# Kernel tuning notes

Measured on AMD Instinct MI355X. Metric: run time of the kernel, lower is better.

The kernel has to match this reference:

```python
import jax, jax.numpy as jnp
import numpy as np

B, C, D, H = 128, 8, 1024, 8
K_RANGE = (2, 3, 4, 5)


def setup_inputs() -> dict:
    key = jax.random.key(0)
    ks = jax.random.split(key, 10)
    s = 0.02
    return {
        "x": jax.random.normal(ks[0], (B, D), jnp.float32),
        # per-K prototype groups, shape (nb_classes, K, embed_dim) as in get_prototype_group()
        "p2": jax.random.normal(ks[1], (C, 2, D), jnp.float32),
        "p3": jax.random.normal(ks[2], (C, 3, D), jnp.float32),
        "p4": jax.random.normal(ks[3], (C, 4, D), jnp.float32),
        "p5": jax.random.normal(ks[4], (C, 5, D), jnp.float32),
        # per-class attention Block params (stacked over class axis)
        "ln_g": jnp.ones((C, D), jnp.float32),
        "ln_b": jnp.zeros((C, D), jnp.float32),
        "w_qkv": jax.random.normal(ks[5], (C, 3 * D, D), jnp.float32) * s,
        "b_qkv": jnp.zeros((C, 3 * D), jnp.float32),
        "w_proj": jax.random.normal(ks[6], (C, D, D), jnp.float32) * s,
        "b_proj": jnp.zeros((C, D), jnp.float32),
        # cls head
        "w_cls": jax.random.normal(ks[7], (C, D), jnp.float32) * s,
        "b_cls": jnp.zeros((C,), jnp.float32),
    }


def _proto_group(x, pg):
    """x: (B,D); pg: (C,K,D). Returns nearest proto (B,D), per-sample class group (B,K,D), class ids (B,)."""
    Cc, K, d = pg.shape
    flat = pg.reshape(Cc * K, d)
    # squared L2 distances (argmin identical to torch.cdist p=2 argmin)
    d2 = (jnp.sum(x * x, axis=1, keepdims=True)
          - 2.0 * (x @ flat.T)
          + jnp.sum(flat * flat, axis=1))
    idx = jnp.argmin(d2, axis=1)          # (B,)
    cls = idx // K                        # (B,)
    return flat[idx], pg[cls], cls


def _vicreg(x, nearest, proto_space, sim_c=25.0, std_c=25.0, cov_c=1.0):
    # sim: pull x toward its nearest prototype in every K-group
    repr_loss = jnp.mean((x[:, None, :] - nearest) ** 2)
    # std over batch of prototype space, unbiased var, eps=1e-4
    std = jnp.sqrt(jnp.var(proto_space, axis=0, ddof=1) + 1e-4)   # (S,D)
    std_loss = jnp.mean(jax.nn.relu(1.0 - std))
    # covariance of centered flattened prototype space
    ps = proto_space - jnp.mean(proto_space, axis=0)
    P = ps.reshape(-1, ps.shape[-1])                              # (B*S, D)
    cov = P.T @ P / (P.shape[0] - 1)
    cov_loss = ((cov ** 2).sum() - (jnp.diagonal(cov) ** 2).sum()) / ps.shape[-1]
    return sim_c * repr_loss + std_c * std_loss + cov_c * cov_loss


def _forward(x, p2, p3, p4, p5, ln_g, ln_b, w_qkv, b_qkv, w_proj, b_proj, w_cls, b_cls):
    groups = (p2, p3, p4, p5)
    nearest_list, space_list, cls = [], [], None
    for pg in groups:
        n, sp, cls = _proto_group(x, pg)   # cls kept from LAST group, as in torch code
        nearest_list.append(n)
        space_list.append(sp)
    nearest = jnp.stack(nearest_list, axis=1)     # (B, len(K_range), D)
    proto_space = jnp.concatenate(space_list, 1)  # (B, sum(K_range), D)

    vcr = _vicreg(x, nearest, proto_space)

    # per-class attention Block: LayerNorm -> MHA -> residual, vectorized over class axis c
    S = proto_space.shape[1]
    mu = proto_space.mean(-1, keepdims=True)
    var = proto_space.var(-1, keepdims=True)
    xn = (proto_space - mu) * jax.lax.rsqrt(var + 1e-5)               # (B,S,D)
    h = xn[None] * ln_g[:, None, None, :] + ln_b[:, None, None, :]    # (C,B,S,D)

    qkv = jnp.einsum('cbsd,cfd->cbsf', h, w_qkv) + b_qkv[:, None, None, :]
    dh = D // H
    qkv = qkv.reshape(C, B, S, 3, H, dh).transpose(3, 0, 1, 4, 2, 5)  # (3,C,B,H,S,dh)
    q, k, v = qkv[0] * (dh ** -0.5), qkv[1], qkv[2]
    attn = jax.nn.softmax(jnp.einsum('cbhqe,cbhke->cbhqk', q, k), axis=-1)
    o = jnp.einsum('cbhqk,cbhke->cbhqe', attn, v)                     # (C,B,H,S,dh)
    o = o.transpose(0, 1, 3, 2, 4).reshape(C, B, S, D)
    out = jnp.einsum('cbsd,ced->cbse', o, w_proj) + b_proj[:, None, None, :]
    attended = proto_space[None] + out                                # (C,B,S,D)

    # route each sample through the block of its (last-group) assigned class
    cond = attended[cls, jnp.arange(B)]                               # (B,S,D)
    cond = cond / jnp.maximum(jnp.linalg.norm(cond, axis=2, keepdims=True), 1e-12)
    pooled = cond.mean(1)                                             # (B,D)
    logits = pooled @ w_cls.T + b_cls
    return logits, vcr


def reference(x, p2, p3, p4, p5, ln_g, ln_b, w_qkv, b_qkv, w_proj, b_proj, w_cls, b_cls):
    return _forward(x, p2, p3, p4, p5, ln_g, ln_b, w_qkv, b_qkv, w_proj, b_proj, w_cls, b_cls)
```

## Files before the change

kernel.cpp:

```cpp
#include <hip/hip_runtime.h>
#include <math.h>

#define NB 128
#define ND 1024
#define NS 14
#define NDH 128

typedef float f32x4 __attribute__((ext_vector_type(4)));
typedef short bf16x8 __attribute__((ext_vector_type(8)));
typedef unsigned int u32x4 __attribute__((ext_vector_type(4)));

__device__ __forceinline__ unsigned short f2bf(float v) {
  unsigned int u = __builtin_bit_cast(unsigned int, v);
  return (unsigned short)((u + 0x7FFFu + ((u >> 16) & 1u)) >> 16);
}
__device__ __forceinline__ float bf2f(unsigned short u) {
  return __builtin_bit_cast(float, (unsigned int)u << 16);
}

__device__ __forceinline__ bf16x8 pack_bv(float4 w0, float4 w1) {
  unsigned int u0, u1, u2, u3;
  asm("v_cvt_pk_bf16_f32 %0, %1, %2" : "=v"(u0) : "v"(w0.x), "v"(w0.y));
  asm("v_cvt_pk_bf16_f32 %0, %1, %2" : "=v"(u1) : "v"(w0.z), "v"(w0.w));
  asm("v_cvt_pk_bf16_f32 %0, %1, %2" : "=v"(u2) : "v"(w1.x), "v"(w1.y));
  asm("v_cvt_pk_bf16_f32 %0, %1, %2" : "=v"(u3) : "v"(w1.z), "v"(w1.w));
  u32x4 u = {u0, u1, u2, u3};
  return __builtin_bit_cast(bf16x8, u);
}

__device__ __forceinline__ void s_decomp(int s, int& g, int& k) {
  if (s < 2)      { g = 0; k = s; }
  else if (s < 5) { g = 1; k = s - 2; }
  else if (s < 9) { g = 2; k = s - 5; }
  else            { g = 3; k = s - 9; }
}
__device__ __forceinline__ const float* grp_ptr(int g, const float* p2, const float* p3,
                                                const float* p4, const float* p5) {
  return g == 0 ? p2 : g == 1 ? p3 : g == 2 ? p4 : p5;
}
__device__ __forceinline__ int grp_base(int g) { return g == 0 ? 0 : g == 1 ? 16 : g == 2 ? 40 : 72; }
__device__ __forceinline__ int grp_k(int g) { return g + 2; }

__global__ __launch_bounds__(256) void k_ln_assign(
    const float* __restrict__ x,
    const float* __restrict__ p2, const float* __restrict__ p3,
    const float* __restrict__ p4, const float* __restrict__ p5,
    const float* __restrict__ ln_g, const float* __restrict__ ln_b,
    const float* __restrict__ w_proj, unsigned short* __restrict__ wpf,
    unsigned short* __restrict__ hbf2, float* __restrict__ pall,
    int* __restrict__ cls, int* __restrict__ rows_g, float* __restrict__ minv)
{
  int bid = blockIdx.x, t = threadIdx.x;
  if (bid >= 240) {
    int idxT = (bid - 240) * 256 + t;
    int c = idxT >> 17;
    int rem = idxT & 131071;
    int col = rem >> 7, kq = rem & 127;
    const float* src = w_proj + (((size_t)c * 1024 + col) << 10) + kq * 8;
    float4 w0 = *(const float4*)(src);
    float4 w1 = *(const float4*)(src + 4);
    bf16x8 v = pack_bv(w0, w1);
    size_t dst = ((((size_t)c * 64 + (col >> 4)) * 32 + (kq >> 2)) << 9)
               + ((kq & 3) * 16 + (col & 15)) * 8;
    *(bf16x8*)(wpf + dst) = v;
    return;
  }
  __shared__ __align__(16) float xs[ND];
  float4* xs4 = (float4*)xs;
  if (bid < 112) {
    int r = bid;
    const float* pp; int idx;
    if (r < 16)      { pp = p2; idx = r; }
    else if (r < 40) { pp = p3; idx = r - 16; }
    else if (r < 72) { pp = p4; idx = r - 40; }
    else             { pp = p5; idx = r - 72; }
    const float4* row4 = (const float4*)(pp + (size_t)idx * ND);
    float4 v = row4[t];
    xs4[t] = v;
    float s1 = v.x + v.y + v.z + v.w;
    float s2 = v.x * v.x + v.y * v.y + v.z * v.z + v.w * v.w;
    __shared__ float ra[256], rb[256];
    ra[t] = s1; rb[t] = s2; __syncthreads();
    for (int o = 128; o > 0; o >>= 1) { if (t < o) { ra[t] += ra[t + o]; rb[t] += rb[t + o]; } __syncthreads(); }
    __shared__ float mu, rstd;
    if (t == 0) {
      float m = ra[0] * (1.f / 1024.f);
      float var = rb[0] * (1.f / 1024.f) - m * m;
      mu = m; rstd = rsqrtf(var + 1e-5f);
    }
    __syncthreads();
    ((float4*)(pall + (size_t)r * ND))[t] = xs4[t];
    float4 xv = xs4[t];
    float nx = (xv.x - mu) * rstd, ny = (xv.y - mu) * rstd,
          nz = (xv.z - mu) * rstd, nw = (xv.w - mu) * rstd;
    int d0 = t * 4;
    int m = r >> 4, rr = r & 15;
    int kblk = d0 >> 5, qq = (d0 >> 3) & 3, e0 = d0 & 7;
    size_t fidx = (size_t)kblk * 3584 + m * 512 + (qq * 16 + rr) * 8 + e0;
#pragma unroll
    for (int c = 0; c < 8; ++c) {
      float4 g = ((const float4*)(ln_g + (size_t)c * ND))[t];
      float4 bb = ((const float4*)(ln_b + (size_t)c * ND))[t];
      ushort4 u;
      u.x = f2bf(nx * g.x + bb.x); u.y = f2bf(ny * g.y + bb.y);
      u.z = f2bf(nz * g.z + bb.z); u.w = f2bf(nw * g.w + bb.w);
      *(ushort4*)&hbf2[(size_t)c * 114688 + fidx] = u;
    }
  } else {
    int b = bid - 112;
    __shared__ float d2s[112];
    __shared__ int cls_s[4];
    const float4* xg4 = (const float4*)(x + (size_t)b * ND);
    xs4[t] = xg4[t];
    __syncthreads();
    int j = t >> 1, half = t & 1;
    if (j < 112) {
      const float* pp; int idx;
      if (j < 16)      { pp = p2; idx = j; }
      else if (j < 40) { pp = p3; idx = j - 16; }
      else if (j < 72) { pp = p4; idx = j - 40; }
      else             { pp = p5; idx = j - 72; }
      const float4* pr4 = (const float4*)(pp + (size_t)idx * ND);
      float acc = 0.f;
      int d0 = half * 128;
#pragma unroll 8
      for (int d = d0; d < d0 + 128; ++d) {
        float4 a = xs4[d], p = pr4[d];
        float dx = a.x - p.x, dy = a.y - p.y, dz = a.z - p.z, dw = a.w - p.w;
        acc += dx * dx + dy * dy + dz * dz + dw * dw;
      }
      acc += __shfl_xor(acc, 1, 2);
      if (half == 0) d2s[j] = acc;
    }
    __syncthreads();
    if (t < 4) {
      int base = grp_base(t), kg = grp_k(t), cnt = 8 * kg;
      float mv = d2s[base]; int mi = 0;
      for (int jj = 1; jj < cnt; ++jj) { float v = d2s[base + jj]; if (v < mv) { mv = v; mi = jj; } }
      int c = mi / kg;
      cls[b * 4 + t] = c; cls_s[t] = c;
      minv[b * 4 + t] = mv;
    }
    __syncthreads();
    if (t < NS) {
      int g, k; s_decomp(t, g, k);
      rows_g[b * NS + t] = grp_base(g) + cls_s[g] * grp_k(g) + k;
    }
  }
}

__global__ __launch_bounds__(256, 4) void k_qkv_prep(
    const unsigned short* __restrict__ hbf2, const float* __restrict__ w_qkv,
    const float* __restrict__ b_qkv, unsigned short* __restrict__ qkv_bf,
    const int* __restrict__ cls, const float* __restrict__ minv,
    int* __restrict__ counts, int* __restrict__ ccnt, int* __restrict__ order,
    int* __restrict__ posof, int* __restrict__ chunkidx, int* __restrict__ chunk_c,
    int* __restrict__ chunk_lo, int* __restrict__ chunkN, float* __restrict__ scal)
{
  __shared__ __align__(16) char smem[32768];
  int bid = blockIdx.x, t = threadIdx.x;
  if (bid == 0) {
    __shared__ int cnt_s[32];
    __shared__ int cc_s[8];
    __shared__ float red[128];
    if (t < 32) cnt_s[t] = 0;
    if (t < 8) cc_s[t] = 0;
    if (t < 4) scal[t] = 0.f;
    __syncthreads();
    if (t < 128) {
      int c3;
#pragma unroll
      for (int g = 0; g < 4; ++g) {
        int c = cls[t * 4 + g];
        atomicAdd(&cnt_s[g * 8 + c], 1);
        if (g == 3) c3 = c;
      }
      int pos = atomicAdd(&cc_s[c3], 1);
      order[c3 * 128 + pos] = t;
      posof[t] = pos;
      red[t] = minv[t * 4 + 0] + minv[t * 4 + 1] + minv[t * 4 + 2] + minv[t * 4 + 3];
    }
    __syncthreads();
    for (int o = 64; o > 0; o >>= 1) { if (t < o) red[t] += red[t + o]; __syncthreads(); }
    if (t == 0) {
      scal[0] = red[0];
      int T = 0;
      for (int c = 0; c < 8; ++c) {
        chunkidx[c] = T;
        int nch = (cc_s[c] + 15) >> 4;
        for (int j = 0; j < nch; ++j) { chunk_c[T] = c; chunk_lo[T] = j * 16; ++T; }
      }
      chunkN[0] = T;
    }
    if (t < 32) counts[t] = cnt_s[t];
    if (t < 8) ccnt[t] = cc_s[t];
    return;
  }
  int qb = bid - 1;
  int c = qb / 192, xb = qb - c * 192;
  int col0 = xb * 16;
  unsigned short* Wl = (unsigned short*)smem;
  {
    const float* Wbase = w_qkv + ((size_t)c * 3072 + col0) * ND;
    int k0 = t * 4;
    int ksq = t >> 6, kblk = (t >> 3) & 7, qq = (t >> 1) & 3, e0 = (t & 1) * 4;
    int sw = ((kblk & 3) << 2) + qq;
    int ebase = ((ksq * 8 + kblk) * 64 + qq * 16) * 8 + e0;
#pragma unroll
    for (int j = 0; j < 16; ++j) {
      float4 w = *(const float4*)(Wbase + (size_t)j * ND + k0);
      unsigned int u0, u1;
      asm("v_cvt_pk_bf16_f32 %0, %1, %2" : "=v"(u0) : "v"(w.x), "v"(w.y));
      asm("v_cvt_pk_bf16_f32 %0, %1, %2" : "=v"(u1) : "v"(w.z), "v"(w.w));
      unsigned int* dst = (unsigned int*)&Wl[ebase + (j ^ sw) * 8];
      dst[0] = u0; dst[1] = u1;
    }
  }
  __syncthreads();
  int lane = t & 63, ks = t >> 6;
  int r16 = lane & 15, q = lane >> 4;
  const unsigned short* Hp = hbf2 + (size_t)c * 114688 + (size_t)(ks * 8) * 3584 + lane * 8;
  f32x4 acc[7] = {};
#pragma unroll
  for (int i = 0; i < 8; ++i) {
    int sr = ((i & 3) << 2) + q;
    bf16x8 bv = *(const bf16x8*)&Wl[(((ks * 8 + i) * 64) + q * 16 + (r16 ^ sr)) * 8];
    const unsigned short* hk = Hp + (size_t)i * 3584;
#pragma unroll
    for (int m = 0; m < 7; ++m) {
      bf16x8 av = *(const bf16x8*)(hk + m * 512);
      acc[m] = __builtin_amdgcn_mfma_f32_16x16x32_bf16(av, bv, acc[m], 0, 0, 0);
    }
  }
  __syncthreads();
  float* lred = (float*)smem;
  if (ks) {
#pragma unroll
    for (int m = 0; m < 7; ++m)
      *(f32x4*)&lred[((ks - 1) * 7 + m) * 256 + lane * 4] = acc[m];
  }
  __syncthreads();
  if (ks == 0) {
    int col = col0 + r16;
    float bq = b_qkv[(size_t)c * 3072 + col];
#pragma unroll
    for (int m = 0; m < 7; ++m) {
      f32x4 s0 = acc[m];
#pragma unroll
      for (int sk = 0; sk < 3; ++sk)
        s0 += *(const f32x4*)&lred[(sk * 7 + m) * 256 + lane * 4];
#pragma unroll
      for (int r = 0; r < 4; ++r) {
        int row = m * 16 + q * 4 + r;
        qkv_bf[((size_t)c * 112 + row) * 3072 + col] = f2bf(s0[r] + bq);
      }
    }
  }
}

__global__ __launch_bounds__(256) void k_attn_stats(
    const unsigned short* __restrict__ qkv_bf, const int* __restrict__ cls,
    const int* __restrict__ rows_g, const int* __restrict__ posof,
    const int* __restrict__ chunkidx, unsigned short* __restrict__ obf2,
    const float* __restrict__ p2, const float* __restrict__ p3,
    const float* __restrict__ p4, const float* __restrict__ p5,
    const int* __restrict__ counts, float* __restrict__ M, float* __restrict__ scal)
{
  int bid = blockIdx.x, t = threadIdx.x;
  if (bid < 1024) {
    __shared__ __align__(16) float qs[NS * NDH], ks2[NS * NDH], vs[NS * NDH];
    __shared__ float sc[NS * NS];
    __shared__ int rg[NS];
    int h = bid & 7, b = bid >> 3;
    if (t < NS) rg[t] = rows_g[b * NS + t];
    __syncthreads();
    int cp = cls[b * 4 + 3];
    int pos = posof[b];
    size_t gbase = (size_t)(chunkidx[cp] + (pos >> 4)) * 229376;
    int slot = pos & 15;
    const float scale = 0.08838834764831843f;
    for (int i = t; i < NS * 32; i += 256) {
      int s = i >> 5, e4 = (i & 31) * 4;
      size_t base = ((size_t)cp * 112 + rg[s]) * 3072 + h * NDH + e4;
      ushort4 uq = *(const ushort4*)&qkv_bf[base];
      ushort4 uk = *(const ushort4*)&qkv_bf[base + 1024];
      ushort4 uv = *(const ushort4*)&qkv_bf[base + 2048];
      int o = s * NDH + e4;
      qs[o]     = bf2f(uq.x) * scale; qs[o + 1] = bf2f(uq.y) * scale;
      qs[o + 2] = bf2f(uq.z) * scale; qs[o + 3] = bf2f(uq.w) * scale;
      ks2[o]     = bf2f(uk.x); ks2[o + 1] = bf2f(uk.y);
      ks2[o + 2] = bf2f(uk.z); ks2[o + 3] = bf2f(uk.w);
      vs[o]     = bf2f(uv.x); vs[o + 1] = bf2f(uv.y);
      vs[o + 2] = bf2f(uv.z); vs[o + 3] = bf2f(uv.w);
    }
    __syncthreads();
    if (t < NS * NS) {
      int si = t / NS, sj = t - (t / NS) * NS;
      const float4* qa = (const float4*)&qs[si * NDH];
      const float4* kb = (const float4*)&ks2[sj * NDH];
      float acc = 0.f;
#pragma unroll 8
      for (int e4 = 0; e4 < 32; ++e4) {
        float4 a = qa[e4], k4 = kb[e4];
        acc += a.x * k4.x + a.y * k4.y + a.z * k4.z + a.w * k4.w;
      }
      sc[t] = acc;
    }
    __syncthreads();
    if (t < NS) {
      float mx = -1e30f;
      for (int j = 0; j < NS; ++j) mx = fmaxf(mx, sc[t * NS + j]);
      float e_[NS]; float sum = 0.f;
      for (int j = 0; j < NS; ++j) { float e = expf(sc[t * NS + j] - mx); e_[j] = e; sum += e; }
      float inv = 1.f / sum;
      for (int j = 0; j < NS; ++j) sc[t * NS + j] = e_[j] * inv;
    }
    __syncthreads();
    for (int i = t; i < NS * 32; i += 256) {
      int s = i >> 5, e4 = i & 31;
      float4 a = {0.f, 0.f, 0.f, 0.f};
#pragma unroll
      for (int j = 0; j < NS; ++j) {
        float w = sc[s * NS + j];
        float4 v4 = ((const float4*)&vs[j * NDH])[e4];
        a.x += w * v4.x; a.y += w * v4.y; a.z += w * v4.z; a.w += w * v4.w;
      }
      int row = slot * 14 + s;
      int m = row >> 4, r16 = row & 15;
      int d0 = h * NDH + e4 * 4;
      int kblk = d0 >> 5, qq = (d0 >> 3) & 3, e0 = d0 & 7;
      ushort4 u; u.x = f2bf(a.x); u.y = f2bf(a.y); u.z = f2bf(a.z); u.w = f2bf(a.w);
      *(ushort4*)&obf2[gbase + (size_t)kblk * 7168 + m * 512 + (qq * 16 + r16) * 8 + e0] = u;
    }
  } else {
    int idx = (bid - 1024) * 256 + t;
    int s = idx >> 10, d = idx & 1023;
    int g, k; s_decomp(s, g, k);
    const float* pp = grp_ptr(g, p2, p3, p4, p5);
    int kg = grp_k(g);
    float vc[8], nc[8];
    float sum = 0.f, sumsq = 0.f;
#pragma unroll
    for (int c = 0; c < 8; ++c) {
      float v = pp[((size_t)(c * kg + k)) * ND + d];
      float n = (float)counts[g * 8 + c];
      vc[c] = v; nc[c] = n;
      sum += n * v; sumsq += n * v * v;
    }
    float mean = sum * (1.f / 128.f);
    float var = (sumsq - 128.f * mean * mean) * (1.f / 127.f);
    float sd = sqrtf(var + 1e-4f);
#pragma unroll
    for (int c = 0; c < 8; ++c)
      M[((size_t)(s * 8 + c)) * ND + d] = sqrtf(nc[c] * (1.f / 1791.f)) * (vc[c] - mean);
    float part = fmaxf(1.f - sd, 0.f);
    __shared__ float red[256];
    red[t] = part; __syncthreads();
    for (int o = 128; o > 0; o >>= 1) { if (t < o) red[t] += red[t + o]; __syncthreads(); }
    if (t == 0) atomicAdd(&scal[1], red[0]);
  }
}

__global__ __launch_bounds__(512) void k_proj_gram(
    const unsigned short* __restrict__ obf2, const unsigned short* __restrict__ wpf,
    const int* __restrict__ order,
    const int* __restrict__ ccnt, const int* __restrict__ chunk_c,
    const int* __restrict__ chunk_lo, const int* __restrict__ chunkN,
    const int* __restrict__ rows_g,
    const float* __restrict__ b_proj,
    const float* __restrict__ pall, float* __restrict__ att,
    const float* __restrict__ M, float* __restrict__ scal)
{
  int bid = blockIdx.x, t = threadIdx.x;
  if (bid < 960) {
    int g = bid / 64, xb = bid - g * 64;
    if (g >= chunkN[0]) return;
    __shared__ __align__(16) float lred[3 * 2 * 7 * 256];
    __shared__ int sid_s[16];
    int c = chunk_c[g], lo = chunk_lo[g];
    int cnt = ccnt[c];
    int nb = cnt - lo; if (nb > 16) nb = 16;
    int lane = t & 63, wid = t >> 6;
    int rh = wid & 1, ks = wid >> 1;
    if (t < 16) sid_s[t] = order[c * 128 + lo + ((t < nb) ? t : nb - 1)];
    int r16 = lane & 15, q = lane >> 4;
    int col = xb * 16 + r16;
    const unsigned short* Wf = wpf + ((((size_t)c * 64 + xb) * 32 + ks * 8) << 9) + lane * 8;
    const unsigned short* Ap = obf2 + (size_t)g * 229376 + (size_t)(ks * 8) * 7168 + rh * 3584 + lane * 8;
    f32x4 acc[7] = {};
#pragma unroll
    for (int i = 0; i < 8; ++i) {
      bf16x8 bv = *(const bf16x8*)(Wf + (size_t)i * 512);
      const unsigned short* ak = Ap + (size_t)i * 7168;
#pragma unroll
      for (int m = 0; m < 7; ++m) {
        bf16x8 av = *(const bf16x8*)(ak + m * 512);
        acc[m] = __builtin_amdgcn_mfma_f32_16x16x32_bf16(av, bv, acc[m], 0, 0, 0);
      }
    }
    if (ks) {
#pragma unroll
      for (int m = 0; m < 7; ++m)
        *(f32x4*)&lred[(((ks - 1) * 2 + rh) * 7 + m) * 256 + lane * 4] = acc[m];
    }
    __syncthreads();
    if (ks == 0) {
      float bp = b_proj[(size_t)c * ND + col];
#pragma unroll
      for (int m = 0; m < 7; ++m) {
        f32x4 a1 = *(const f32x4*)&lred[((0 * 2 + rh) * 7 + m) * 256 + lane * 4];
        f32x4 a2 = *(const f32x4*)&lred[((1 * 2 + rh) * 7 + m) * 256 + lane * 4];
        f32x4 a3 = *(const f32x4*)&lred[((2 * 2 + rh) * 7 + m) * 256 + lane * 4];
#pragma unroll
        for (int r = 0; r < 4; ++r) {
          int row = rh * 112 + m * 16 + q * 4 + r;
          int slot = row / 14, s = row - slot * 14;
          if (slot < nb) {
            int b = sid_s[slot];
            float res = pall[(size_t)rows_g[b * NS + s] * ND + col];
            att[((size_t)b * NS + s) * ND + col] = acc[m][r] + a1[r] + a2[r] + a3[r] + bp + res;
          }
        }
      }
    }
  } else if (bid < 1072) {
    int r = bid - 960;
    __shared__ __align__(16) float mi[ND];
    __shared__ float red2[128];
    float4* mi4 = (float4*)mi;
    const float4* src4 = (const float4*)(M + (size_t)r * ND);
    if (t < 256) mi4[t] = src4[t];
    if (t < 128) red2[t] = 0.f;
    __syncthreads();
    int j = t >> 2, qd = t & 3;
    float p = 0.f;
    if (j < 112) {
      const float4* mj4 = (const float4*)(M + (size_t)j * ND);
      float acc = 0.f;
#pragma unroll 8
      for (int d = qd * 64; d < qd * 64 + 64; ++d) {
        float4 a = mi4[d], b = mj4[d];
        acc += a.x * b.x + a.y * b.y + a.z * b.z + a.w * b.w;
      }
      acc += __shfl_xor(acc, 1, 4);
      acc += __shfl_xor(acc, 2, 4);
      p = acc * acc;
    }
    if (qd == 0 && j < 112) red2[j] = p;
    __syncthreads();
    for (int o = 64; o > 0; o >>= 1) { if (t < o) red2[t] += red2[t + o]; __syncthreads(); }
    if (t == 0) atomicAdd(&scal[2], red2[0]);
  } else {
    int d = (bid - 1072) * 512 + t;
    float tsum = 0.f;
    for (int r = 0; r < 112; ++r) { float v = M[(size_t)r * ND + d]; tsum += v * v; }
    __shared__ float red3[512];
    red3[t] = tsum * tsum; __syncthreads();
    for (int o = 256; o > 0; o >>= 1) { if (t < o) red3[t] += red3[t + o]; __syncthreads(); }
    if (t == 0) atomicAdd(&scal[3], red3[0]);
  }
}

__global__ __launch_bounds__(256) void k_final(
    const float* __restrict__ att, const float* __restrict__ w_cls,
    const float* __restrict__ b_cls, const float* __restrict__ scal,
    float* __restrict__ out)
{
  int b = blockIdx.x, t = threadIdx.x;
  __shared__ __align__(16) float as[NS * ND];
  __shared__ float wred[NS][4];
  __shared__ float inv[NS];
  __shared__ __align__(16) float pooled[ND];
  int lane = t & 63, w = t >> 6;
#pragma unroll
  for (int s = 0; s < NS; ++s) {
    float4 v = ((const float4*)(att + ((size_t)b * NS + s) * ND))[t];
    ((float4*)&as[s * ND])[t] = v;
    float p = v.x * v.x + v.y * v.y + v.z * v.z + v.w * v.w;
#pragma unroll
    for (int o = 32; o > 0; o >>= 1) p += __shfl_xor(p, o, 64);
    if (lane == 0) wred[s][w] = p;
  }
  __syncthreads();
  if (t < NS) {
    float s2 = wred[t][0] + wred[t][1] + wred[t][2] + wred[t][3];
    inv[t] = 1.f / fmaxf(sqrtf(s2), 1e-12f);
  }
  __syncthreads();
  float4 pa = {0.f, 0.f, 0.f, 0.f};
#pragma unroll
  for (int s = 0; s < NS; ++s) {
    float iv = inv[s];
    float4 v = ((const float4*)&as[s * ND])[t];
    pa.x += iv * v.x; pa.y += iv * v.y; pa.z += iv * v.z; pa.w += iv * v.w;
  }
  const float k14 = 1.f / 14.f;
  pa.x *= k14; pa.y *= k14; pa.z *= k14; pa.w *= k14;
  ((float4*)pooled)[t] = pa;
  __syncthreads();
  int c = t >> 5, l = t & 31;
  float acc = 0.f;
#pragma unroll
  for (int k = 0; k < 8; ++k) {
    int i4 = l + k * 32;
    float4 p4 = ((const float4*)pooled)[i4];
    float4 wc = ((const float4*)(w_cls + (size_t)c * ND))[i4];
    acc += p4.x * wc.x + p4.y * wc.y + p4.z * wc.z + p4.w * wc.w;
  }
  for (int o = 16; o > 0; o >>= 1) acc += __shfl_down(acc, o, 32);
  if (l == 0) out[b * 8 + c] = acc + b_cls[c];
  if (b == 0 && t == 0) {
    float repr = scal[0] * (1.f / (128.f * 4.f * 1024.f));
    float stdl = scal[1] * (1.f / 14336.f);
    float covl = (scal[2] - scal[3]) * (1.f / 1024.f);
    out[1024] = 25.f * repr + 25.f * stdl + covl;
  }
}

extern "C" void kernel_launch(void* const* d_in, const int* in_sizes, int n_in,
                              void* d_out, int out_size, void* d_ws, size_t ws_size,
                              hipStream_t stream) {
  const float* x      = (const float*)d_in[0];
  const float* p2     = (const float*)d_in[1];
  const float* p3     = (const float*)d_in[2];
  const float* p4     = (const float*)d_in[3];
  const float* p5     = (const float*)d_in[4];
  const float* ln_g   = (const float*)d_in[5];
  const float* ln_b   = (const float*)d_in[6];
  const float* w_qkv  = (const float*)d_in[7];
  const float* b_qkv  = (const float*)d_in[8];
  const float* w_proj = (const float*)d_in[9];
  const float* b_proj = (const float*)d_in[10];
  const float* w_cls  = (const float*)d_in[11];
  const float* b_cls  = (const float*)d_in[12];
  float* out = (float*)d_out;
  char* ws = (char*)d_ws;

  float* scal      = (float*)(ws + 0);
  int*   counts    = (int*)(ws + 64);
  int*   ccnt      = (int*)(ws + 192);
  int*   cls       = (int*)(ws + 256);
  int*   rows_g    = (int*)(ws + 2304);
  int*   order     = (int*)(ws + 9472);
  float* minv      = (float*)(ws + 13568);
  int*   posof     = (int*)(ws + 15616);
  int*   chunkidx  = (int*)(ws + 16128);
  int*   chunk_c   = (int*)(ws + 16160);
  int*   chunk_lo  = (int*)(ws + 16224);
  int*   chunkN    = (int*)(ws + 16288);
  float* pall      = (float*)(ws + 16384);
  unsigned short* hbf2 = (unsigned short*)(ws + 475136);
  unsigned short* qkvb = (unsigned short*)(ws + 2310144);
  unsigned short* obf2 = (unsigned short*)(ws + 7815168);
  float* att       = (float*)(ws + 15155200);
  float* M         = (float*)(ws + 22495232);
  unsigned short* wpf = (unsigned short*)(ws + 22953984);

  k_ln_assign<<<4336, 256, 0, stream>>>(x, p2, p3, p4, p5, ln_g, ln_b, w_proj, wpf,
                                        hbf2, pall, cls, rows_g, minv);
  k_qkv_prep<<<1537, 256, 0, stream>>>(hbf2, w_qkv, b_qkv, qkvb, cls, minv,
                                       counts, ccnt, order, posof, chunkidx, chunk_c, chunk_lo, chunkN, scal);
  k_attn_stats<<<1080, 256, 0, stream>>>(qkvb, cls, rows_g, posof, chunkidx, obf2,
                                         p2, p3, p4, p5, counts, M, scal);
  k_proj_gram<<<1074, 512, 0, stream>>>(obf2, wpf, order, ccnt, chunk_c, chunk_lo, chunkN, rows_g,
                                        b_proj, pall, att, M, scal);
  k_final<<<128, 256, 0, stream>>>(att, w_cls, b_cls, scal, out);
}
```

Measured before the change: 124.8 us.

## Pre-pack w_qkv to bf16 MFMA layout in first kernel, drop LDS staging

Adds 12288 blocks to the first kernel that convert w_qkv to bf16 in an MFMA-fragment layout in workspace, when the workspace is large enough. The QKV GEMM then loads B fragments directly from global memory instead of converting and staging them through shared memory. That removes one __syncthreads and most of the LDS use, and raises the occupancy hint to 5. A fallback path converts w_qkv directly from fp32 global memory. The cost is an extra bf16 write and read of the weights and reuse of workspace regions shared with obf2.

```diff
diff --git a/kernel.cpp b/kernel.cpp
--- a/kernel.cpp
+++ b/kernel.cpp
@@ -47,10 +47,25 @@
     const float* __restrict__ p4, const float* __restrict__ p5,
     const float* __restrict__ ln_g, const float* __restrict__ ln_b,
     const float* __restrict__ w_proj, unsigned short* __restrict__ wpf,
+    const float* __restrict__ w_qkv, unsigned short* __restrict__ wqf,
     unsigned short* __restrict__ hbf2, float* __restrict__ pall,
     int* __restrict__ cls, int* __restrict__ rows_g, float* __restrict__ minv)
 {
   int bid = blockIdx.x, t = threadIdx.x;
+  if (bid >= 4336) {
+    int idxT = (bid - 4336) * 256 + t;
+    int c = idxT / 393216;
+    int rem = idxT - c * 393216;
+    int col = rem >> 7, kq = rem & 127;
+    const float* src = w_qkv + (((size_t)c * 3072 + col) << 10) + kq * 8;
+    float4 w0 = *(const float4*)(src);
+    float4 w1 = *(const float4*)(src + 4);
+    bf16x8 v = pack_bv(w0, w1);
+    size_t dst = ((((size_t)c * 192 + (col >> 4)) * 32 + (kq >> 2)) << 9)
+               + ((kq & 3) * 16 + (col & 15)) * 8;
+    *(bf16x8*)(wqf + dst) = v;
+    return;
+  }
   if (bid >= 240) {
     int idxT = (bid - 240) * 256 + t;
     int c = idxT >> 17;
@@ -149,15 +164,16 @@
   }
 }
 
-__global__ __launch_bounds__(256, 4) void k_qkv_prep(
+__global__ __launch_bounds__(256, 5) void k_qkv_prep(
     const unsigned short* __restrict__ hbf2, const float* __restrict__ w_qkv,
+    const unsigned short* __restrict__ wqf, int use_wqf,
     const float* __restrict__ b_qkv, unsigned short* __restrict__ qkv_bf,
     const int* __restrict__ cls, const float* __restrict__ minv,
     int* __restrict__ counts, int* __restrict__ ccnt, int* __restrict__ order,
     int* __restrict__ posof, int* __restrict__ chunkidx, int* __restrict__ chunk_c,
     int* __restrict__ chunk_lo, int* __restrict__ chunkN, float* __restrict__ scal)
 {
-  __shared__ __align__(16) char smem[32768];
+  __shared__ __align__(16) float lred[3 * 7 * 256];
   int bid = blockIdx.x, t = threadIdx.x;
   if (bid == 0) {
     __shared__ int cnt_s[32];
@@ -198,42 +214,38 @@
   }
   int qb = bid - 1;
   int c = qb / 192, xb = qb - c * 192;
-  int col0 = xb * 16;
-  unsigned short* Wl = (unsigned short*)smem;
-  {
-    const float* Wbase = w_qkv + ((size_t)c * 3072 + col0) * ND;
-    int k0 = t * 4;
-    int ksq = t >> 6, kblk = (t >> 3) & 7, qq = (t >> 1) & 3, e0 = (t & 1) * 4;
-    int sw = ((kblk & 3) << 2) + qq;
-    int ebase = ((ksq * 8 + kblk) * 64 + qq * 16) * 8 + e0;
-#pragma unroll
-    for (int j = 0; j < 16; ++j) {
-      float4 w = *(const float4*)(Wbase + (size_t)j * ND + k0);
-      unsigned int u0, u1;
-      asm("v_cvt_pk_bf16_f32 %0, %1, %2" : "=v"(u0) : "v"(w.x), "v"(w.y));
-      asm("v_cvt_pk_bf16_f32 %0, %1, %2" : "=v"(u1) : "v"(w.z), "v"(w.w));
-      unsigned int* dst = (unsigned int*)&Wl[ebase + (j ^ sw) * 8];
-      dst[0] = u0; dst[1] = u1;
-    }
-  }
-  __syncthreads();
   int lane = t & 63, ks = t >> 6;
   int r16 = lane & 15, q = lane >> 4;
+  int col = xb * 16 + r16;
   const unsigned short* Hp = hbf2 + (size_t)c * 114688 + (size_t)(ks * 8) * 3584 + lane * 8;
   f32x4 acc[7] = {};
-#pragma unroll
-  for (int i = 0; i < 8; ++i) {
-    int sr = ((i & 3) << 2) + q;
-    bf16x8 bv = *(const bf16x8*)&Wl[(((ks * 8 + i) * 64) + q * 16 + (r16 ^ sr)) * 8];
-    const unsigned short* hk = Hp + (size_t)i * 3584;
-#pragma unroll
-    for (int m = 0; m < 7; ++m) {
-      bf16x8 av = *(const bf16x8*)(hk + m * 512);
-      acc[m] = __builtin_amdgcn_mfma_f32_16x16x32_bf16(av, bv, acc[m], 0, 0, 0);
-    }
-  }
-  __syncthreads();
-  float* lred = (float*)smem;
+  if (use_wqf) {
+    const unsigned short* Wf = wqf + ((((size_t)c * 192 + xb) * 32 + ks * 8) << 9) + lane * 8;
+#pragma unroll
+    for (int i = 0; i < 8; ++i) {
+      bf16x8 bv = *(const bf16x8*)(Wf + (size_t)i * 512);
+      const unsigned short* hk = Hp + (size_t)i * 3584;
+#pragma unroll
+      for (int m = 0; m < 7; ++m) {
+        bf16x8 av = *(const bf16x8*)(hk + m * 512);
+        acc[m] = __builtin_amdgcn_mfma_f32_16x16x32_bf16(av, bv, acc[m], 0, 0, 0);
+      }
+    }
+  } else {
+    const float* Wp = w_qkv + ((size_t)c * 3072 + col) * ND + ks * 256 + q * 8;
+#pragma unroll
+    for (int i = 0; i < 8; ++i) {
+      float4 w0 = *(const float4*)(Wp + i * 32);
+      float4 w1 = *(const float4*)(Wp + i * 32 + 4);
+      bf16x8 bv = pack_bv(w0, w1);
+      const unsigned short* hk = Hp + (size_t)i * 3584;
+#pragma unroll
+      for (int m = 0; m < 7; ++m) {
+        bf16x8 av = *(const bf16x8*)(hk + m * 512);
+        acc[m] = __builtin_amdgcn_mfma_f32_16x16x32_bf16(av, bv, acc[m], 0, 0, 0);
+      }
+    }
+  }
   if (ks) {
 #pragma unroll
     for (int m = 0; m < 7; ++m)
@@ -241,7 +253,6 @@
   }
   __syncthreads();
   if (ks == 0) {
-    int col = col0 + r16;
     float bq = b_qkv[(size_t)c * 3072 + col];
 #pragma unroll
     for (int m = 0; m < 7; ++m) {
@@ -551,14 +562,29 @@
   float* pall      = (float*)(ws + 16384);
   unsigned short* hbf2 = (unsigned short*)(ws + 475136);
   unsigned short* qkvb = (unsigned short*)(ws + 2310144);
-  unsigned short* obf2 = (unsigned short*)(ws + 7815168);
-  float* att       = (float*)(ws + 15155200);
-  float* M         = (float*)(ws + 22495232);
-  unsigned short* wpf = (unsigned short*)(ws + 22953984);
-
-  k_ln_assign<<<4336, 256, 0, stream>>>(x, p2, p3, p4, p5, ln_g, ln_b, w_proj, wpf,
-                                        hbf2, pall, cls, rows_g, minv);
-  k_qkv_prep<<<1537, 256, 0, stream>>>(hbf2, w_qkv, b_qkv, qkvb, cls, minv,
+
+  const size_t NEED = 74924032ULL;
+  int use_wqf = (ws_size >= NEED) ? 1 : 0;
+
+  unsigned short* obf2; float* att; float* M; unsigned short* wpf; unsigned short* wqf;
+  if (use_wqf) {
+    wqf  = (unsigned short*)(ws + 7815168);
+    obf2 = (unsigned short*)(ws + 7815168);
+    M    = (float*)(ws + 15155200);
+    att  = (float*)(ws + 15613952);
+    wpf  = (unsigned short*)(ws + 58146816);
+  } else {
+    obf2 = (unsigned short*)(ws + 7815168);
+    att  = (float*)(ws + 15155200);
+    M    = (float*)(ws + 22495232);
+    wpf  = (unsigned short*)(ws + 22953984);
+    wqf  = (unsigned short*)(ws + 22953984);
+  }
+
+  int grid1 = use_wqf ? 16624 : 4336;
+  k_ln_assign<<<grid1, 256, 0, stream>>>(x, p2, p3, p4, p5, ln_g, ln_b, w_proj, wpf,
+                                         w_qkv, wqf, hbf2, pall, cls, rows_g, minv);
+  k_qkv_prep<<<1537, 256, 0, stream>>>(hbf2, w_qkv, wqf, use_wqf, b_qkv, qkvb, cls, minv,
                                        counts, ccnt, order, posof, chunkidx, chunk_c, chunk_lo, chunkN, scal);
   k_attn_stats<<<1080, 256, 0, stream>>>(qkvb, cls, rows_g, posof, chunkidx, obf2,
                                          p2, p3, p4, p5, counts, M, scal);
```

New measurement: 130.8 us. +4.9%, slower.

## Stage w_qkv via direct global-to-LDS loads and retile w_proj conversion through LDS

Applied to the files above, without the earlier changes.

The QKV projection kernel now loads fp32 weight rows straight into shared memory with global_load_lds using a rotated layout, and converts them to bf16 at use time instead of converting through registers before a barrier. Shared memory doubles to 64KB and the occupancy hint drops to 2 blocks per SM. The w_proj bf16 repacking is reworked so each block handles a 16x512 tile and transposes it through LDS, giving coalesced writes with far fewer blocks. The aim is lower weight-load latency and fewer instructions, at the cost of lower occupancy and extra conversion work inside the MFMA loop.

```diff
diff --git a/kernel.cpp b/kernel.cpp
--- a/kernel.cpp
+++ b/kernel.cpp
@@ -16,6 +16,12 @@
 }
 __device__ __forceinline__ float bf2f(unsigned short u) {
   return __builtin_bit_cast(float, (unsigned int)u << 16);
+}
+
+__device__ __forceinline__ void gl_lds16(const void* g, void* l) {
+  __builtin_amdgcn_global_load_lds(
+      (const __attribute__((address_space(1))) void*)g,
+      (__attribute__((address_space(3))) void*)l, 16, 0, 0);
 }
 
 __device__ __forceinline__ bf16x8 pack_bv(float4 w0, float4 w1) {
@@ -51,21 +57,32 @@
     int* __restrict__ cls, int* __restrict__ rows_g, float* __restrict__ minv)
 {
   int bid = blockIdx.x, t = threadIdx.x;
+  __shared__ __align__(16) unsigned short tl2[8192];
   if (bid >= 240) {
-    int idxT = (bid - 240) * 256 + t;
-    int c = idxT >> 17;
-    int rem = idxT & 131071;
-    int col = rem >> 7, kq = rem & 127;
-    const float* src = w_proj + (((size_t)c * 1024 + col) << 10) + kq * 8;
-    float4 w0 = *(const float4*)(src);
-    float4 w1 = *(const float4*)(src + 4);
-    bf16x8 v = pack_bv(w0, w1);
-    size_t dst = ((((size_t)c * 64 + (col >> 4)) * 32 + (kq >> 2)) << 9)
-               + ((kq & 3) * 16 + (col & 15)) * 8;
-    *(bf16x8*)(wpf + dst) = v;
+    int i = bid - 240;
+    int c = i >> 7, r2 = i & 127, cb = r2 >> 1, kb2 = r2 & 1;
+    const float* Wb = w_proj + (((size_t)c * 1024 + cb * 16) << 10) + kb2 * 512;
+    int r = t >> 4, kk = (t & 15) * 8, g = t & 15;
+    float4 a0[4], a1[4];
+#pragma unroll
+    for (int j = 0; j < 4; ++j) {
+      a0[j] = *(const float4*)(Wb + (size_t)r * ND + j * 128 + kk);
+      a1[j] = *(const float4*)(Wb + (size_t)r * ND + j * 128 + kk + 4);
+    }
+#pragma unroll
+    for (int j = 0; j < 4; ++j) {
+      bf16x8 v = pack_bv(a0[j], a1[j]);
+      *(bf16x8*)&tl2[j * 2048 + (g * 16 + (r ^ g)) * 8] = v;
+    }
+    __syncthreads();
+    size_t B = ((size_t)((c * 64 + cb) * 32 + kb2 * 16)) << 9;
+    int gr = t >> 4, rr = t & 15;
+#pragma unroll
+    for (int j = 0; j < 4; ++j)
+      *(bf16x8*)&wpf[B + j * 2048 + t * 8] = *(const bf16x8*)&tl2[j * 2048 + (gr * 16 + (rr ^ gr)) * 8];
     return;
   }
-  __shared__ __align__(16) float xs[ND];
+  float* xs = (float*)tl2;
   float4* xs4 = (float4*)xs;
   if (bid < 112) {
     int r = bid;
@@ -149,7 +166,7 @@
   }
 }
 
-__global__ __launch_bounds__(256, 4) void k_qkv_prep(
+__global__ __launch_bounds__(256, 2) void k_qkv_prep(
     const unsigned short* __restrict__ hbf2, const float* __restrict__ w_qkv,
     const float* __restrict__ b_qkv, unsigned short* __restrict__ qkv_bf,
     const int* __restrict__ cls, const float* __restrict__ minv,
@@ -157,12 +174,12 @@
     int* __restrict__ posof, int* __restrict__ chunkidx, int* __restrict__ chunk_c,
     int* __restrict__ chunk_lo, int* __restrict__ chunkN, float* __restrict__ scal)
 {
-  __shared__ __align__(16) char smem[32768];
+  __shared__ __align__(16) char smem[65536];
   int bid = blockIdx.x, t = threadIdx.x;
   if (bid == 0) {
-    __shared__ int cnt_s[32];
-    __shared__ int cc_s[8];
-    __shared__ float red[128];
+    int* cnt_s = (int*)smem;
+    int* cc_s  = (int*)(smem + 128);
+    float* red = (float*)(smem + 192);
     if (t < 32) cnt_s[t] = 0;
     if (t < 8) cc_s[t] = 0;
     if (t < 4) scal[t] = 0.f;
@@ -181,7 +198,7 @@
       red[t] = minv[t * 4 + 0] + minv[t * 4 + 1] + minv[t * 4 + 2] + minv[t * 4 + 3];
     }
     __syncthreads();
-    for (int o = 64; o > 0; o >>= 1) { if (t < o) red[t] += red[t + o]; __syncthreads(); }
+    for (int o = 64; o > 0; o >>= 1) { if (t < o && t < 128) red[t] += red[t + o]; __syncthreads(); }
     if (t == 0) {
       scal[0] = red[0];
       int T = 0;
@@ -198,33 +215,31 @@
   }
   int qb = bid - 1;
   int c = qb / 192, xb = qb - c * 192;
-  int col0 = xb * 16;
-  unsigned short* Wl = (unsigned short*)smem;
-  {
-    const float* Wbase = w_qkv + ((size_t)c * 3072 + col0) * ND;
-    int k0 = t * 4;
-    int ksq = t >> 6, kblk = (t >> 3) & 7, qq = (t >> 1) & 3, e0 = (t & 1) * 4;
-    int sw = ((kblk & 3) << 2) + qq;
-    int ebase = ((ksq * 8 + kblk) * 64 + qq * 16) * 8 + e0;
-#pragma unroll
-    for (int j = 0; j < 16; ++j) {
-      float4 w = *(const float4*)(Wbase + (size_t)j * ND + k0);
-      unsigned int u0, u1;
-      asm("v_cvt_pk_bf16_f32 %0, %1, %2" : "=v"(u0) : "v"(w.x), "v"(w.y));
-      asm("v_cvt_pk_bf16_f32 %0, %1, %2" : "=v"(u1) : "v"(w.z), "v"(w.w));
-      unsigned int* dst = (unsigned int*)&Wl[ebase + (j ^ sw) * 8];
-      dst[0] = u0; dst[1] = u1;
-    }
-  }
-  __syncthreads();
   int lane = t & 63, ks = t >> 6;
   int r16 = lane & 15, q = lane >> 4;
+  int col = xb * 16 + r16;
+  {
+    const char* Wrow = (const char*)w_qkv + ((size_t)(c * 3072 + xb * 16) << 12) + ks * 1024;
+    char* ldsb = smem + ks * 16384;
+    int l16 = lane * 16;
+#pragma unroll
+    for (int j = 0; j < 16; ++j) {
+      int off = (l16 + j * 16) & 1023;
+      gl_lds16(Wrow + ((size_t)j << 12) + off, ldsb + j * 1024);
+    }
+    asm volatile("s_waitcnt vmcnt(0)" ::: "memory");
+    __builtin_amdgcn_sched_barrier(0);
+  }
   const unsigned short* Hp = hbf2 + (size_t)c * 114688 + (size_t)(ks * 8) * 3584 + lane * 8;
+  const char* slot = smem + ks * 16384 + r16 * 1024;
+  int rot = r16 * 16;
   f32x4 acc[7] = {};
 #pragma unroll
   for (int i = 0; i < 8; ++i) {
-    int sr = ((i & 3) << 2) + q;
-    bf16x8 bv = *(const bf16x8*)&Wl[(((ks * 8 + i) * 64) + q * 16 + (r16 ^ sr)) * 8];
+    int o = i * 128 + q * 32;
+    float4 w0 = *(const float4*)(slot + ((o - rot) & 1023));
+    float4 w1 = *(const float4*)(slot + ((o + 16 - rot) & 1023));
+    bf16x8 bv = pack_bv(w0, w1);
     const unsigned short* hk = Hp + (size_t)i * 3584;
 #pragma unroll
     for (int m = 0; m < 7; ++m) {
@@ -241,7 +256,6 @@
   }
   __syncthreads();
   if (ks == 0) {
-    int col = col0 + r16;
     float bq = b_qkv[(size_t)c * 3072 + col];
 #pragma unroll
     for (int m = 0; m < 7; ++m) {
@@ -556,7 +570,7 @@
   float* M         = (float*)(ws + 22495232);
   unsigned short* wpf = (unsigned short*)(ws + 22953984);
 
-  k_ln_assign<<<4336, 256, 0, stream>>>(x, p2, p3, p4, p5, ln_g, ln_b, w_proj, wpf,
+  k_ln_assign<<<1264, 256, 0, stream>>>(x, p2, p3, p4, p5, ln_g, ln_b, w_proj, wpf,
                                         hbf2, pall, cls, rows_g, minv);
   k_qkv_prep<<<1537, 256, 0, stream>>>(hbf2, w_qkv, b_qkv, qkvb, cls, minv,
                                        counts, ccnt, order, posof, chunkidx, chunk_c, chunk_lo, chunkN, scal);
```

Result: no change. 124.6 us (-0.2%).
